# Performance work log

Measured on AMD Instinct MI355X. Metric: run time of the kernel, lower is better.

## Reference

```python
import jax, jax.numpy as jnp
import numpy as np

N = 50000          # nodes
E = 800000         # edges (avg degree 16)
IN_DIM = 64        # input feature dim
HEADS = 8          # heads in hidden layers
T = 3              # num edge types
NUM_CLASSES = 16   # output layer: 1 head, hidden = num_classes
SLOPE = 0.2        # LeakyReLU negative slope


def typed_linear(x, etype, W):
    # x: [E, din], W: [T, din, dout] -> per-edge-type linear (grouped GEMM)
    out = jnp.zeros((x.shape[0], W.shape[2]), dtype=x.dtype)
    for t in range(W.shape[0]):  # small fixed loop over edge types
        out = out + jnp.where((etype == t)[:, None], x @ W[t], jnp.zeros((), x.dtype))
    return out


def edge_softmax(scores, dst, n):
    # segmented softmax over incoming edges of each dst node; scores: [E, H]
    m = jax.ops.segment_max(scores, dst, num_segments=n)
    e = jnp.exp(scores - m[dst])
    s = jax.ops.segment_sum(e, dst, num_segments=n)
    return e / s[dst]


def hetsann_conv(x, src, dst, etype, W, a_l, a_r, heads, res, act, n):
    ne = src.shape[0]
    m = x[src]                                   # copy_u: gather src features to edges
    feat = typed_linear(m, etype, W)             # [E, heads*d]
    d = feat.shape[1] // heads
    h_l = typed_linear(feat, etype, a_l).reshape(ne, heads, d).sum(-1)  # [E, H]
    h_r = typed_linear(feat, etype, a_r).reshape(ne, heads, d).sum(-1)  # [E, H]
    att = jax.nn.leaky_relu(h_l + h_r, SLOPE)    # [E, H]
    alpha = edge_softmax(att, dst, n)            # [E, H]
    # attention-weighted messages, scatter-summed to dst (HetSANN eq. 5)
    msg = (feat.reshape(ne, heads, d) * alpha[:, :, None]).reshape(ne, heads * d)
    out = jax.ops.segment_sum(msg, dst, num_segments=n)  # [N, heads*d]
    if res is not None:
        w, b = res
        out = out + x @ w + b
    if act:
        out = jax.nn.elu(out)
    return out


def setup_inputs() -> dict:
    key = jax.random.key(0)
    ks = jax.random.split(key, 14)
    s = 1.0 / np.sqrt(IN_DIM)
    s2 = 1.0 / np.sqrt(NUM_CLASSES)
    return {
        "x": jax.random.normal(ks[0], (N, IN_DIM), dtype=jnp.float32),
        "src": jax.random.randint(ks[1], (E,), 0, N),
        "dst": jax.random.randint(ks[2], (E,), 0, N),
        "ntype": jax.random.randint(ks[3], (N,), 0, T),
        "etype": jax.random.randint(ks[4], (E,), 0, T),
        # layer 0: TypedLinear(64 -> 64), heads=8
        "W1": jax.random.normal(ks[5], (T, IN_DIM, IN_DIM), dtype=jnp.float32) * s,
        "al1": jax.random.normal(ks[6], (T, IN_DIM, IN_DIM), dtype=jnp.float32) * s,
        "ar1": jax.random.normal(ks[7], (T, IN_DIM, IN_DIM), dtype=jnp.float32) * s,
        # layer 1 (output): TypedLinear(64 -> 16), heads=1, residual Linear(64 -> 16)
        "W2": jax.random.normal(ks[8], (T, IN_DIM, NUM_CLASSES), dtype=jnp.float32) * s,
        "al2": jax.random.normal(ks[9], (T, NUM_CLASSES, NUM_CLASSES), dtype=jnp.float32) * s2,
        "ar2": jax.random.normal(ks[10], (T, NUM_CLASSES, NUM_CLASSES), dtype=jnp.float32) * s2,
        "res_w": jax.random.normal(ks[11], (IN_DIM, NUM_CLASSES), dtype=jnp.float32) * s,
        "res_b": jax.random.normal(ks[12], (NUM_CLASSES,), dtype=jnp.float32) * 0.01,
    }


def reference(x, src, dst, ntype, etype, W1, al1, ar1, W2, al2, ar2, res_w, res_b):
    # layer 0: 8 heads, no residual, ELU activation (dropout=0 -> identity)
    h = hetsann_conv(x, src, dst, etype, W1, al1, ar1, HEADS, None, True, N)
    # output layer: 1 head, hidden=num_classes, residual, no activation
    h = hetsann_conv(h, src, dst, etype, W2, al2, ar2, 1, (res_w, res_b), False, N)
    # dgl.mean_nodes over the single graph
    return h.mean(axis=0)  # [NUM_CLASSES]
```

## Files before the change

kernel.cpp:

```cpp
#include <hip/hip_runtime.h>
#include <hip/hip_bf16.h>

typedef unsigned int u32;
typedef unsigned short u16;
typedef unsigned char u8;

#define NN 50000
#define EE 800000
#define TT 3
#define NBUCK 196
#define BSTRIDE 8192
#define P1_CHUNK 4096

#define OFF_BCNT   1728
#define OFF_OPART  1984
#define OFF_ROWPTR 52756
#define OFF_CW1    102760
#define OFF_CW2    117096
#define OFF_PSRC   153016
#define OFF_PK1    953024
#define OFF_TMP    953024
#define OFF_PK2    953024
#define OFF_XT     5753024
#define OFF_H      5753024

__device__ __forceinline__ float bf2f(u32 u) {
    union { u32 i; float f; } v; v.i = u << 16; return v.f;
}
__device__ __forceinline__ u32 f2bf(float f) {
    union { float f; u32 i; } v; v.f = f;
    return (v.i + 0x7fffu + ((v.i >> 16) & 1u)) >> 16;
}

__global__ void weights_k(const float* __restrict__ W1, const float* __restrict__ al1,
                          const float* __restrict__ ar1, const float* __restrict__ W2,
                          const float* __restrict__ al2, const float* __restrict__ ar2,
                          const float* __restrict__ res_w, float* __restrict__ ws) {
    __shared__ float a1c[64][8];
    __shared__ float a2c[16];
    int t = blockIdx.x;
    int tid = threadIdx.x;
    {
        int k2 = tid >> 3, hh = tid & 7;
        float s = 0.f;
#pragma unroll
        for (int j = 0; j < 8; ++j) {
            int idx = t * 4096 + k2 * 64 + hh * 8 + j;
            s += al1[idx] + ar1[idx];
        }
        a1c[k2][hh] = s;
    }
    if (tid < 16) {
        float s = 0.f;
#pragma unroll
        for (int j = 0; j < 16; ++j) {
            int idx = t * 256 + tid * 16 + j;
            s += al2[idx] + ar2[idx];
        }
        a2c[tid] = s;
    }
    __syncthreads();
    for (int q = tid; q < 4096; q += 512) {
        int k = q >> 6, j = q & 63;
        ws[OFF_CW1 + k * 224 + 64 * t + j] = W1[t * 4096 + q];
    }
    {
        int k = tid >> 3, h = tid & 7;
        float s = 0.f;
#pragma unroll
        for (int k2 = 0; k2 < 64; ++k2)
            s += W1[t * 4096 + k * 64 + k2] * a1c[k2][h];
        ws[OFF_CW1 + k * 224 + 192 + 8 * t + h] = s;
    }
    for (int q = tid; q < 1024; q += 512) {
        int k = q >> 4, j = q & 15;
        ws[OFF_CW2 + k * 68 + 16 * t + j] = W2[t * 1024 + q];
    }
    if (tid < 64) {
        float s = 0.f;
#pragma unroll
        for (int k2 = 0; k2 < 16; ++k2)
            s += W2[t * 1024 + tid * 16 + k2] * a2c[k2];
        ws[OFF_CW2 + tid * 68 + 48 + t] = s;
    }
    if (t == 0) {
        for (int q = tid; q < 1024; q += 512) {
            int k = q >> 4, j = q & 15;
            ws[OFF_CW2 + k * 68 + 51 + j] = res_w[q];
        }
        { int k = tid >> 3; ws[OFF_CW1 + k * 224 + 216 + (tid & 7)] = 0.f; }
        if (tid < 64) ws[OFF_CW2 + tid * 68 + 67] = 0.f;
    }
}

__global__ __launch_bounds__(256) void sort_p1(const int* __restrict__ src, const int* __restrict__ dst,
                        const int* __restrict__ etype, int* wsi) {
    __shared__ u32 Est[P1_CHUNK];
    __shared__ u8 Bst[P1_CHUNK];
    __shared__ int hist[NBUCK], base[NBUCK];
    int tid = threadIdx.x;
    int e0 = blockIdx.x * P1_CHUNK;
    int cnt = EE - e0; if (cnt > P1_CHUNK) cnt = P1_CHUNK;
    for (int i = tid; i < NBUCK; i += 256) hist[i] = 0;
    __syncthreads();
    for (int i = tid; i < cnt; i += 256) {
        int e = e0 + i;
        int s = src[e], d = dst[e], t = etype[e];
        int b = d >> 8;
        Est[i] = (u32)s | ((u32)t << 16) | ((u32)(d & 255) << 18);
        Bst[i] = (u8)b;
        atomicAdd(&hist[b], 1);
    }
    __syncthreads();
    for (int i = tid; i < NBUCK; i += 256) {
        int h = hist[i];
        base[i] = h ? atomicAdd(wsi + OFF_BCNT + i, h) : 0;
        hist[i] = 0;
    }
    __syncthreads();
    for (int i = tid; i < cnt; i += 256) {
        int b = Bst[i];
        int idx = base[b] + atomicAdd(&hist[b], 1);
        wsi[OFF_TMP + b * BSTRIDE + idx] = (int)Est[i];
    }
}

__global__ __launch_bounds__(256) void sort_p2(int* wsi) {
    __shared__ int cnt[256], sd[256], lrpx[256];
    __shared__ int gb_s, nb_s;
    int b = blockIdx.x;
    int tid = threadIdx.x;
    int v0 = (tid < NBUCK) ? wsi[OFF_BCNT + tid] : 0;
    sd[tid] = v0;
    __syncthreads();
    for (int o = 1; o < 256; o <<= 1) {
        int u = (tid >= o) ? sd[tid - o] : 0;
        __syncthreads();
        sd[tid] += u;
        __syncthreads();
    }
    if (tid == 0) {
        int nb = wsi[OFF_BCNT + b];
        gb_s = sd[b] - nb;
        nb_s = nb;
        if (b == 0) wsi[OFF_ROWPTR + NN] = EE;
    }
    __syncthreads();
    int gbase = gb_s, nb = nb_s;
    cnt[tid] = 0;
    __syncthreads();
    const int* tmp = wsi + OFF_TMP + b * BSTRIDE;
    for (int i = tid; i < nb; i += 256) {
        int e = tmp[i];
        atomicAdd(&cnt[(e >> 18) & 255], 1);
    }
    __syncthreads();
    int v = cnt[tid];
    sd[tid] = v;
    __syncthreads();
    for (int o = 1; o < 256; o <<= 1) {
        int u = (tid >= o) ? sd[tid - o] : 0;
        __syncthreads();
        sd[tid] += u;
        __syncthreads();
    }
    int ex = sd[tid] - v;
    lrpx[tid] = ex;
    int d = b * 256 + tid;
    if (d < NN) wsi[OFF_ROWPTR + d] = gbase + ex;
    cnt[tid] = 0;
    __syncthreads();
    for (int i = tid; i < nb; i += 256) {
        int e = tmp[i];
        int dres = (e >> 18) & 255;
        int slot = gbase + lrpx[dres] + atomicAdd(&cnt[dres], 1);
        wsi[OFF_PSRC + slot] = (e & 0xFFFF) | (((e >> 16) & 3) << 20);
    }
}

__global__ __launch_bounds__(256) void xt_k(const float* __restrict__ x, float* __restrict__ ws) {
    __shared__ alignas(16) float Xs[64 * 65];
    int tid = threadIdx.x;
    int n0 = blockIdx.x * 64;
    {
        const float4* xg = (const float4*)(x + (size_t)n0 * 64);
        for (int q = tid; q < 1024; q += 256) {
            int row = q >> 4;
            float4 v = (n0 + row < NN) ? xg[q] : make_float4(0.f, 0.f, 0.f, 0.f);
            *(float4*)(Xs + row * 65 + (q & 15) * 4) = v;
        }
    }
    __syncthreads();
    int lane = tid & 63, cg = tid >> 6;
    int n = n0 + lane;
    if (n < NN) {
#pragma unroll
        for (int i = 0; i < 16; ++i) {
            int c = cg * 16 + i;
            ws[OFF_XT + (size_t)c * 50000 + n] = Xs[lane * 65 + c];
        }
    }
}

__global__ __launch_bounds__(512) void gemm_f(const float* __restrict__ xt, const float* __restrict__ cw,
                       float* __restrict__ ws) {
    int tid = threadIdx.x;
    int wave = __builtin_amdgcn_readfirstlane(tid >> 6);
    int lane = tid & 63;
    int n0 = blockIdx.x * 64;
    int n = n0 + lane;
    int nc = n < NN ? n : NN - 1;
    int cbase = wave * 28;
    float acc[28];
#pragma unroll
    for (int i = 0; i < 28; ++i) acc[i] = 0.f;
    float wA[28], wB[28];
#pragma unroll
    for (int j = 0; j < 28; ++j) wA[j] = cw[cbase + j];
    float xA = xt[nc];
    float xB = xt[(size_t)50000 + nc];
    for (int k = 0; k < 64; k += 2) {
#pragma unroll
        for (int j = 0; j < 28; ++j) wB[j] = cw[(k + 1) * 224 + cbase + j];
        float xvA = xA;
        if (k + 2 < 64) xA = xt[(size_t)(k + 2) * 50000 + nc];
#pragma unroll
        for (int j = 0; j < 28; ++j) acc[j] = fmaf(xvA, wA[j], acc[j]);
        if (k + 2 < 64) {
#pragma unroll
            for (int j = 0; j < 28; ++j) wA[j] = cw[(k + 2) * 224 + cbase + j];
        }
        float xvB = xB;
        if (k + 2 < 64) xB = xt[(size_t)(k + 3) * 50000 + nc];
#pragma unroll
        for (int j = 0; j < 28; ++j) acc[j] = fmaf(xvB, wB[j], acc[j]);
    }
    if (n < NN) {
        u32* row = (u32*)ws + OFF_PK1 + (size_t)n * 96;
#pragma unroll
        for (int g = 0; g < 7; ++g) {
            int col = cbase + 4 * g;
            float v0 = acc[4*g], v1 = acc[4*g+1], v2 = acc[4*g+2], v3 = acc[4*g+3];
            if (col < 192) {
                int t = col >> 6, ci = col & 63;
                int dw = __builtin_amdgcn_cvt_pk_fp8_f32(v0, v1, 0, false);
                dw = __builtin_amdgcn_cvt_pk_fp8_f32(v2, v3, dw, true);
                row[t * 32 + (ci >> 2)] = (u32)dw;
            } else if (col < 216) {
                int jj = col - 192;
                int t = jj >> 3, rem = jj & 7;
                v0 = v0 > 0.f ? v0 : 0.2f * v0;
                v1 = v1 > 0.f ? v1 : 0.2f * v1;
                v2 = v2 > 0.f ? v2 : 0.2f * v2;
                v3 = v3 > 0.f ? v3 : 0.2f * v3;
                row[t * 32 + 16 + (rem >> 1)]     = f2bf(__expf(v0)) | (f2bf(__expf(v1)) << 16);
                row[t * 32 + 16 + (rem >> 1) + 1] = f2bf(__expf(v2)) | (f2bf(__expf(v3)) << 16);
            }
        }
    }
}

__global__ __launch_bounds__(256) void agg1(const int* __restrict__ wsi, float* __restrict__ ws) {
    int tid = threadIdx.x;
    int wave = tid >> 6, lane = tid & 63;
    int q = lane >> 3;
    int cg = lane & 7;
    int d = blockIdx.x * 4 + wave;
    int epw = cg >> 1;
    int sh_ep = (cg & 1) * 16;
    int start = wsi[OFF_ROWPTR + d], end = wsi[OFF_ROWPTR + d + 1];
    const u32* pk = (const u32*)ws + OFF_PK1;
    const int* psrc = wsi + OFF_PSRC;
    float acc[8];
#pragma unroll
    for (int i = 0; i < 8; ++i) acc[i] = 0.f;
    float den = 0.f;
    int s = start + q;
    u32 f0_c = 0, f1_c = 0, ep_c = 0;
    int p1 = 0;
    bool valid = s < end;
    if (valid) {
        int p = psrc[s];
        int sn = p & 0xFFFFF, t = p >> 20;
        size_t base = (size_t)(sn * 3 + t) * 32;
        uint2 f = *(const uint2*)(pk + base + 2 * cg);
        f0_c = f.x; f1_c = f.y;
        ep_c = pk[base + 16 + epw];
    }
    if (s + 8 < end) p1 = psrc[s + 8];
    while (valid) {
        u32 f0 = f0_c, f1 = f1_c, ep = ep_c;
        bool v1 = s + 8 < end;
        if (v1) {
            int sn = p1 & 0xFFFFF, t = p1 >> 20;
            size_t base = (size_t)(sn * 3 + t) * 32;
            uint2 f = *(const uint2*)(pk + base + 2 * cg);
            f0_c = f.x; f1_c = f.y;
            ep_c = pk[base + 16 + epw];
        }
        if (s + 16 < end) p1 = psrc[s + 16];
        float w = bf2f((ep >> sh_ep) & 0xffffu);
        den += w;
        acc[0] += w * __builtin_amdgcn_cvt_f32_fp8((int)f0, 0);
        acc[1] += w * __builtin_amdgcn_cvt_f32_fp8((int)(f0 >> 8), 0);
        acc[2] += w * __builtin_amdgcn_cvt_f32_fp8((int)(f0 >> 16), 0);
        acc[3] += w * __builtin_amdgcn_cvt_f32_fp8((int)(f0 >> 24), 0);
        acc[4] += w * __builtin_amdgcn_cvt_f32_fp8((int)f1, 0);
        acc[5] += w * __builtin_amdgcn_cvt_f32_fp8((int)(f1 >> 8), 0);
        acc[6] += w * __builtin_amdgcn_cvt_f32_fp8((int)(f1 >> 16), 0);
        acc[7] += w * __builtin_amdgcn_cvt_f32_fp8((int)(f1 >> 24), 0);
        s += 8;
        valid = v1;
    }
#pragma unroll
    for (int i = 0; i < 8; ++i) {
        acc[i] += __shfl_xor(acc[i], 8);
        acc[i] += __shfl_xor(acc[i], 16);
        acc[i] += __shfl_xor(acc[i], 32);
    }
    den += __shfl_xor(den, 8);
    den += __shfl_xor(den, 16);
    den += __shfl_xor(den, 32);
    if (q == 0) {
        float dn = (end > start) ? den : 1.f;
        float o[8];
#pragma unroll
        for (int i = 0; i < 8; ++i) {
            float v = acc[i] / dn;
            o[i] = v > 0.f ? v : __expf(v) - 1.f;
        }
        float* dst = ws + OFF_H + (size_t)d * 64 + cg * 8;
        *(float4*)dst       = make_float4(o[0], o[1], o[2], o[3]);
        *(float4*)(dst + 4) = make_float4(o[4], o[5], o[6], o[7]);
    }
}

__global__ __launch_bounds__(256) void gemm_f2(const float* __restrict__ cw, float* __restrict__ ws) {
    __shared__ alignas(16) float Hs[64 * 65];
    __shared__ float Rs[64][17];
    int tid = threadIdx.x;
    int wave = __builtin_amdgcn_readfirstlane(tid >> 6);
    int lane = tid & 63;
    int n0 = blockIdx.x * 64;
    {
        const float4* hg = (const float4*)(ws + OFF_H + (size_t)n0 * 64);
        for (int q = tid; q < 1024; q += 256) {
            int row = q >> 4;
            float4 v = (n0 + row < NN) ? hg[q] : make_float4(0.f, 0.f, 0.f, 0.f);
            *(float4*)(Hs + row * 65 + (q & 15) * 4) = v;
        }
    }
    __syncthreads();
    int cbase = wave * 17;
    float acc[17];
#pragma unroll
    for (int i = 0; i < 17; ++i) acc[i] = 0.f;
    const float* hrow = Hs + lane * 65;
    float wA[17], wB[17];
#pragma unroll
    for (int j = 0; j < 17; ++j) wA[j] = cw[cbase + j];
    for (int k = 0; k < 64; k += 2) {
#pragma unroll
        for (int j = 0; j < 17; ++j) wB[j] = cw[(k + 1) * 68 + cbase + j];
        float hv = hrow[k];
#pragma unroll
        for (int j = 0; j < 17; ++j) acc[j] = fmaf(hv, wA[j], acc[j]);
        if (k + 2 < 64) {
#pragma unroll
            for (int j = 0; j < 17; ++j) wA[j] = cw[(k + 2) * 68 + cbase + j];
        }
        float hv2 = hrow[k + 1];
#pragma unroll
        for (int j = 0; j < 17; ++j) acc[j] = fmaf(hv2, wB[j], acc[j]);
    }
    int n = n0 + lane;
    u16* pk2u = (u16*)((u32*)ws + OFF_PK2);
#pragma unroll
    for (int i = 0; i < 17; ++i) {
        int col = cbase + i;
        if (col < 48) {
            if (n < NN) {
                int t = col >> 4, c2 = col & 15;
                pk2u[((size_t)n * 3 + t) * 32 + c2] = (u16)f2bf(acc[i]);
            }
        } else if (col < 51) {
            if (n < NN) {
                float v = acc[i]; v = v > 0.f ? v : 0.2f * v;
                ws[OFF_PK2 + ((size_t)n * 3 + (col - 48)) * 16 + 8] = __expf(v);
            }
        } else if (col < 67) {
            Rs[lane][col - 51] = acc[i];
        }
    }
    __syncthreads();
    if (tid < 16) {
        float s = 0.f;
#pragma unroll 8
        for (int r = 0; r < 64; ++r) s += Rs[r][tid];
        atomicAdd(ws + OFF_OPART + (blockIdx.x & 63) * 16 + tid, s);
    }
}

__global__ __launch_bounds__(256) void agg2(const int* __restrict__ wsi, float* __restrict__ ws) {
    __shared__ float outs[4][16];
    int tid = threadIdx.x;
    int wave = tid >> 6, lane = tid & 63;
    int q = lane >> 4, c = lane & 15;
    int d = blockIdx.x * 4 + wave;
    int start = wsi[OFF_ROWPTR + d], end = wsi[OFF_ROWPTR + d + 1];
    const u16* pk2u = (const u16*)((const u32*)ws + OFF_PK2);
    const float* pk2f = ws + OFF_PK2;
    const int* psrc = wsi + OFF_PSRC;
    float acc = 0.f, den = 0.f;
    int s = start + q;
    float w_c = 0.f, m_c = 0.f;
    bool valid = s < end;
    if (valid) {
        int p = psrc[s];
        int sn = p & 0xFFFFF, t = p >> 20;
        size_t r = (size_t)(sn * 3 + t);
        w_c = pk2f[r * 16 + 8];
        m_c = bf2f(pk2u[r * 32 + c]);
    }
    while (valid) {
        float w = w_c, m = m_c;
        int s2 = s + 4;
        bool v2 = s2 < end;
        if (v2) {
            int p = psrc[s2];
            int sn = p & 0xFFFFF, t = p >> 20;
            size_t r = (size_t)(sn * 3 + t);
            w_c = pk2f[r * 16 + 8];
            m_c = bf2f(pk2u[r * 32 + c]);
        }
        den += w;
        acc += w * m;
        s = s2; valid = v2;
    }
    acc += __shfl_xor(acc, 16);
    acc += __shfl_xor(acc, 32);
    den += __shfl_xor(den, 16);
    den += __shfl_xor(den, 32);
    float val = (end > start) ? acc / den : 0.f;
    if (q == 0) outs[wave][c] = val;
    __syncthreads();
    if (tid < 16) {
        float sum = outs[0][tid] + outs[1][tid] + outs[2][tid] + outs[3][tid];
        atomicAdd(ws + OFF_OPART + (blockIdx.x & 63) * 16 + tid, sum);
    }
}

__global__ void final_k(const float* __restrict__ res_b, float* __restrict__ ws, float* __restrict__ out) {
    int c = threadIdx.x;
    if (c < 16) {
        float s = 0.f;
        for (int r = 0; r < 64; ++r) s += ws[OFF_OPART + r * 16 + c];
        out[c] = s * (1.0f / (float)NN) + res_b[c];
    }
}

extern "C" void kernel_launch(void* const* d_in, const int* in_sizes, int n_in,
                              void* d_out, int out_size, void* d_ws, size_t ws_size,
                              hipStream_t stream) {
    const float* x     = (const float*)d_in[0];
    const int*   src   = (const int*)d_in[1];
    const int*   dst   = (const int*)d_in[2];
    const int*   etype = (const int*)d_in[4];
    const float* W1    = (const float*)d_in[5];
    const float* al1   = (const float*)d_in[6];
    const float* ar1   = (const float*)d_in[7];
    const float* W2    = (const float*)d_in[8];
    const float* al2   = (const float*)d_in[9];
    const float* ar2   = (const float*)d_in[10];
    const float* res_w = (const float*)d_in[11];
    const float* res_b = (const float*)d_in[12];
    float* ws = (float*)d_ws;
    int* wsi = (int*)d_ws;
    float* out = (float*)d_out;

    hipMemsetAsync((char*)d_ws + (size_t)OFF_BCNT * 4, 0, (size_t)1280 * 4, stream);
    hipLaunchKernelGGL(weights_k, dim3(TT), dim3(512), 0, stream, W1, al1, ar1, W2, al2, ar2, res_w, ws);
    hipLaunchKernelGGL(sort_p1, dim3((EE + P1_CHUNK - 1) / P1_CHUNK), dim3(256), 0, stream, src, dst, etype, wsi);
    hipLaunchKernelGGL(sort_p2, dim3(NBUCK), dim3(256), 0, stream, wsi);
    hipLaunchKernelGGL(xt_k, dim3((NN + 63) / 64), dim3(256), 0, stream, x, ws);
    hipLaunchKernelGGL(gemm_f, dim3((NN + 63) / 64), dim3(512), 0, stream, ws + OFF_XT, ws + OFF_CW1, ws);
    hipLaunchKernelGGL(agg1, dim3(NN / 4), dim3(256), 0, stream, wsi, ws);
    hipLaunchKernelGGL(gemm_f2, dim3((NN + 63) / 64), dim3(256), 0, stream, ws + OFF_CW2, ws);
    hipLaunchKernelGGL(agg2, dim3(NN / 4), dim3(256), 0, stream, wsi, ws);
    hipLaunchKernelGGL(final_k, dim3(1), dim3(64), 0, stream, res_b, ws, out);
}
```

Measured before the change: 268.8 us.

## Fuse x transpose into layer-1 GEMM and layer-2 GEMM into aggregation epilogue

Removes the separate transpose kernel by staging x rows in shared memory inside gemm_f. It also drops the intermediate hidden-feature buffer and gemm_f2 by computing the layer-2 typed linear, attention exponentials and residual projection directly in agg1's epilogue, using wave shuffles to broadcast each node's 64 hidden values. This saves two kernel launches and a round trip of the N×64 hidden tensor through global memory. In exchange, every lane of agg1 now does 64 FMAs with global weight loads and shuffles per node, and gemm_f reads x from LDS with a padded stride.

New measurement: 399.6 us. 1.49x slower.

```diff
diff --git a/kernel.cpp b/kernel.cpp
--- a/kernel.cpp
+++ b/kernel.cpp
@@ -20,9 +20,7 @@
 #define OFF_PSRC   153016
 #define OFF_PK1    953024
 #define OFF_TMP    953024
-#define OFF_PK2    953024
-#define OFF_XT     5753024
-#define OFF_H      5753024
+#define OFF_PK2N   5753024
 
 __device__ __forceinline__ float bf2f(u32 u) {
     union { u32 i; float f; } v; v.i = u << 16; return v.f;
@@ -178,63 +176,45 @@
     }
 }
 
-__global__ __launch_bounds__(256) void xt_k(const float* __restrict__ x, float* __restrict__ ws) {
+__global__ __launch_bounds__(512) void gemm_f(const float* __restrict__ x, const float* __restrict__ cw,
+                       float* __restrict__ ws) {
     __shared__ alignas(16) float Xs[64 * 65];
     int tid = threadIdx.x;
+    int wave = __builtin_amdgcn_readfirstlane(tid >> 6);
+    int lane = tid & 63;
     int n0 = blockIdx.x * 64;
     {
         const float4* xg = (const float4*)(x + (size_t)n0 * 64);
-        for (int q = tid; q < 1024; q += 256) {
+        for (int q = tid; q < 1024; q += 512) {
             int row = q >> 4;
             float4 v = (n0 + row < NN) ? xg[q] : make_float4(0.f, 0.f, 0.f, 0.f);
             *(float4*)(Xs + row * 65 + (q & 15) * 4) = v;
         }
     }
     __syncthreads();
-    int lane = tid & 63, cg = tid >> 6;
-    int n = n0 + lane;
-    if (n < NN) {
-#pragma unroll
-        for (int i = 0; i < 16; ++i) {
-            int c = cg * 16 + i;
-            ws[OFF_XT + (size_t)c * 50000 + n] = Xs[lane * 65 + c];
-        }
-    }
-}
-
-__global__ __launch_bounds__(512) void gemm_f(const float* __restrict__ xt, const float* __restrict__ cw,
-                       float* __restrict__ ws) {
-    int tid = threadIdx.x;
-    int wave = __builtin_amdgcn_readfirstlane(tid >> 6);
-    int lane = tid & 63;
-    int n0 = blockIdx.x * 64;
-    int n = n0 + lane;
-    int nc = n < NN ? n : NN - 1;
     int cbase = wave * 28;
     float acc[28];
 #pragma unroll
     for (int i = 0; i < 28; ++i) acc[i] = 0.f;
+    const float* xrow = Xs + lane * 65;
     float wA[28], wB[28];
 #pragma unroll
     for (int j = 0; j < 28; ++j) wA[j] = cw[cbase + j];
-    float xA = xt[nc];
-    float xB = xt[(size_t)50000 + nc];
     for (int k = 0; k < 64; k += 2) {
 #pragma unroll
         for (int j = 0; j < 28; ++j) wB[j] = cw[(k + 1) * 224 + cbase + j];
-        float xvA = xA;
-        if (k + 2 < 64) xA = xt[(size_t)(k + 2) * 50000 + nc];
-#pragma unroll
-        for (int j = 0; j < 28; ++j) acc[j] = fmaf(xvA, wA[j], acc[j]);
+        float xv = xrow[k];
+#pragma unroll
+        for (int j = 0; j < 28; ++j) acc[j] = fmaf(xv, wA[j], acc[j]);
         if (k + 2 < 64) {
 #pragma unroll
             for (int j = 0; j < 28; ++j) wA[j] = cw[(k + 2) * 224 + cbase + j];
         }
-        float xvB = xB;
-        if (k + 2 < 64) xB = xt[(size_t)(k + 3) * 50000 + nc];
-#pragma unroll
-        for (int j = 0; j < 28; ++j) acc[j] = fmaf(xvB, wB[j], acc[j]);
-    }
+        float xv2 = xrow[k + 1];
+#pragma unroll
+        for (int j = 0; j < 28; ++j) acc[j] = fmaf(xv2, wB[j], acc[j]);
+    }
+    int n = n0 + lane;
     if (n < NN) {
         u32* row = (u32*)ws + OFF_PK1 + (size_t)n * 96;
 #pragma unroll
@@ -260,7 +240,9 @@
     }
 }
 
-__global__ __launch_bounds__(256) void agg1(const int* __restrict__ wsi, float* __restrict__ ws) {
+__global__ __launch_bounds__(256) void agg1f(const int* __restrict__ wsi, const float* __restrict__ cw2,
+                                             float* __restrict__ ws) {
+    __shared__ float Rs[4][16];
     int tid = threadIdx.x;
     int wave = tid >> 6, lane = tid & 63;
     int q = lane >> 3;
@@ -321,83 +303,43 @@
     den += __shfl_xor(den, 8);
     den += __shfl_xor(den, 16);
     den += __shfl_xor(den, 32);
-    if (q == 0) {
-        float dn = (end > start) ? den : 1.f;
-        float o[8];
+    float dn = (end > start) ? den : 1.f;
+    float h[8];
+#pragma unroll
+    for (int i = 0; i < 8; ++i) {
+        float v = acc[i] / dn;
+        h[i] = v > 0.f ? v : __expf(v) - 1.f;
+    }
+    float a2 = 0.f, a2b = 0.f;
+    bool extra = lane < 3;
+#pragma unroll
+    for (int g = 0; g < 8; ++g) {
+        float hg[8];
+#pragma unroll
+        for (int i = 0; i < 8; ++i) hg[i] = __shfl(h[i], g);
 #pragma unroll
         for (int i = 0; i < 8; ++i) {
-            float v = acc[i] / dn;
-            o[i] = v > 0.f ? v : __expf(v) - 1.f;
-        }
-        float* dst = ws + OFF_H + (size_t)d * 64 + cg * 8;
-        *(float4*)dst       = make_float4(o[0], o[1], o[2], o[3]);
-        *(float4*)(dst + 4) = make_float4(o[4], o[5], o[6], o[7]);
-    }
-}
-
-__global__ __launch_bounds__(256) void gemm_f2(const float* __restrict__ cw, float* __restrict__ ws) {
-    __shared__ alignas(16) float Hs[64 * 65];
-    __shared__ float Rs[64][17];
-    int tid = threadIdx.x;
-    int wave = __builtin_amdgcn_readfirstlane(tid >> 6);
-    int lane = tid & 63;
-    int n0 = blockIdx.x * 64;
-    {
-        const float4* hg = (const float4*)(ws + OFF_H + (size_t)n0 * 64);
-        for (int q = tid; q < 1024; q += 256) {
-            int row = q >> 4;
-            float4 v = (n0 + row < NN) ? hg[q] : make_float4(0.f, 0.f, 0.f, 0.f);
-            *(float4*)(Hs + row * 65 + (q & 15) * 4) = v;
-        }
-    }
-    __syncthreads();
-    int cbase = wave * 17;
-    float acc[17];
-#pragma unroll
-    for (int i = 0; i < 17; ++i) acc[i] = 0.f;
-    const float* hrow = Hs + lane * 65;
-    float wA[17], wB[17];
-#pragma unroll
-    for (int j = 0; j < 17; ++j) wA[j] = cw[cbase + j];
-    for (int k = 0; k < 64; k += 2) {
-#pragma unroll
-        for (int j = 0; j < 17; ++j) wB[j] = cw[(k + 1) * 68 + cbase + j];
-        float hv = hrow[k];
-#pragma unroll
-        for (int j = 0; j < 17; ++j) acc[j] = fmaf(hv, wA[j], acc[j]);
-        if (k + 2 < 64) {
-#pragma unroll
-            for (int j = 0; j < 17; ++j) wA[j] = cw[(k + 2) * 68 + cbase + j];
-        }
-        float hv2 = hrow[k + 1];
-#pragma unroll
-        for (int j = 0; j < 17; ++j) acc[j] = fmaf(hv2, wB[j], acc[j]);
-    }
-    int n = n0 + lane;
-    u16* pk2u = (u16*)((u32*)ws + OFF_PK2);
-#pragma unroll
-    for (int i = 0; i < 17; ++i) {
-        int col = cbase + i;
-        if (col < 48) {
-            if (n < NN) {
-                int t = col >> 4, c2 = col & 15;
-                pk2u[((size_t)n * 3 + t) * 32 + c2] = (u16)f2bf(acc[i]);
-            }
-        } else if (col < 51) {
-            if (n < NN) {
-                float v = acc[i]; v = v > 0.f ? v : 0.2f * v;
-                ws[OFF_PK2 + ((size_t)n * 3 + (col - 48)) * 16 + 8] = __expf(v);
-            }
-        } else if (col < 67) {
-            Rs[lane][col - 51] = acc[i];
-        }
-    }
+            int k = g * 8 + i;
+            a2 = fmaf(hg[i], cw2[k * 68 + lane], a2);
+            if (extra) a2b = fmaf(hg[i], cw2[k * 68 + 64 + lane], a2b);
+        }
+    }
+    u16* pk2u = (u16*)((u32*)ws + OFF_PK2N);
+    float* pk2f = ws + OFF_PK2N;
+    int c = lane;
+    if (c < 48) {
+        pk2u[((size_t)d * 3 + (c >> 4)) * 32 + (c & 15)] = (u16)f2bf(a2);
+    } else if (c < 51) {
+        float v = a2 > 0.f ? a2 : 0.2f * a2;
+        pk2f[((size_t)d * 3 + (c - 48)) * 16 + 8] = __expf(v);
+    } else {
+        Rs[wave][c - 51] = a2;
+    }
+    if (extra) Rs[wave][13 + lane] = a2b;
     __syncthreads();
     if (tid < 16) {
-        float s = 0.f;
-#pragma unroll 8
-        for (int r = 0; r < 64; ++r) s += Rs[r][tid];
-        atomicAdd(ws + OFF_OPART + (blockIdx.x & 63) * 16 + tid, s);
+        float sum = Rs[0][tid] + Rs[1][tid] + Rs[2][tid] + Rs[3][tid];
+        atomicAdd(ws + OFF_OPART + (blockIdx.x & 63) * 16 + tid, sum);
     }
 }
 
@@ -408,8 +350,8 @@
     int q = lane >> 4, c = lane & 15;
     int d = blockIdx.x * 4 + wave;
     int start = wsi[OFF_ROWPTR + d], end = wsi[OFF_ROWPTR + d + 1];
-    const u16* pk2u = (const u16*)((const u32*)ws + OFF_PK2);
-    const float* pk2f = ws + OFF_PK2;
+    const u16* pk2u = (const u16*)((const u32*)ws + OFF_PK2N);
+    const float* pk2f = ws + OFF_PK2N;
     const int* psrc = wsi + OFF_PSRC;
     float acc = 0.f, den = 0.f;
     int s = start + q;
@@ -482,10 +424,8 @@
     hipLaunchKernelGGL(weights_k, dim3(TT), dim3(512), 0, stream, W1, al1, ar1, W2, al2, ar2, res_w, ws);
     hipLaunchKernelGGL(sort_p1, dim3((EE + P1_CHUNK - 1) / P1_CHUNK), dim3(256), 0, stream, src, dst, etype, wsi);
     hipLaunchKernelGGL(sort_p2, dim3(NBUCK), dim3(256), 0, stream, wsi);
-    hipLaunchKernelGGL(xt_k, dim3((NN + 63) / 64), dim3(256), 0, stream, x, ws);
-    hipLaunchKernelGGL(gemm_f, dim3((NN + 63) / 64), dim3(512), 0, stream, ws + OFF_XT, ws + OFF_CW1, ws);
-    hipLaunchKernelGGL(agg1, dim3(NN / 4), dim3(256), 0, stream, wsi, ws);
-    hipLaunchKernelGGL(gemm_f2, dim3((NN + 63) / 64), dim3(256), 0, stream, ws + OFF_CW2, ws);
+    hipLaunchKernelGGL(gemm_f, dim3((NN + 63) / 64), dim3(512), 0, stream, x, ws + OFF_CW1, ws);
+    hipLaunchKernelGGL(agg1f, dim3(NN / 4), dim3(256), 0, stream, wsi, ws + OFF_CW2, ws);
     hipLaunchKernelGGL(agg2, dim3(NN / 4), dim3(256), 0, stream, wsi, ws);
     hipLaunchKernelGGL(final_k, dim3(1), dim3(64), 0, stream, res_b, ws, out);
 }
```
